# Performance work log

Hardware: AMD Instinct MI355X
Metric: run time of the kernel (lower is better)

Reference implementation:

```python
import jax, jax.numpy as jnp
import numpy as np

B, H0, W0, C, NH, WS, SHIFT = 32, 48, 48, 384, 12, 12, 6
N = WS * WS
TAB = 2 * WS - 1  # 23


def _window_partition(x, ws):
    b, h, w, c = x.shape
    x = x.reshape(b, h // ws, ws, w // ws, ws, c)
    return x.transpose(0, 1, 3, 2, 4, 5).reshape(-1, ws, ws, c)


def _window_reverse(win, ws, h, w):
    b = win.shape[0] // (h * w // ws // ws)
    x = win.reshape(b, h // ws, w // ws, ws, ws, -1)
    return x.transpose(0, 1, 3, 2, 4, 5).reshape(b, h, w, -1)


def _ln(y, g, b):
    m = y.mean(-1, keepdims=True)
    v = y.var(-1, keepdims=True)
    return (y - m) * jax.lax.rsqrt(v + 1e-5) * g + b


def setup_inputs() -> dict:
    key = jax.random.key(0)
    ks = jax.random.split(key, 12)
    s = 0.02
    # relative coords table, normalized to [-1, 1]
    rng = np.arange(-(WS - 1), WS, dtype=np.float32) / (WS - 1)
    table = np.stack(np.meshgrid(rng, rng, indexing='ij'), axis=-1)[None]  # (1,23,23,2)
    # relative position index
    ch, cw = np.meshgrid(np.arange(WS), np.arange(WS), indexing='ij')
    coords = np.stack([ch, cw]).reshape(2, -1)
    rel = coords[:, :, None] - coords[:, None, :] + (WS - 1)
    rpi = (rel[0] * TAB + rel[1]).astype(np.int32)  # (N,N)
    # shifted-window attention mask
    img = np.zeros((1, H0, W0, 1), dtype=np.float32)
    cnt = 0
    sl = (slice(0, -WS), slice(-WS, -SHIFT), slice(-SHIFT, None))
    for hs in sl:
        for ws_ in sl:
            img[:, hs, ws_, :] = cnt
            cnt += 1
    mw = img.reshape(1, H0 // WS, WS, W0 // WS, WS, 1).transpose(0, 1, 3, 2, 4, 5).reshape(-1, N)
    diff = mw[:, None, :] - mw[:, :, None]
    attn_mask = np.where(diff != 0, -100.0, 0.0).astype(np.float32)  # (nW,N,N)
    Ch = C * 4
    return {
        'x': jax.random.normal(ks[0], (B, H0 * W0, C), jnp.float32),
        'relative_coords_table': jnp.asarray(table),
        'relative_position_index': jnp.asarray(rpi),
        'attn_mask': jnp.asarray(attn_mask),
        'qkv_w': jax.random.normal(ks[1], (C, 3 * C), jnp.float32) * s,
        'q_bias': jnp.zeros((C,), jnp.float32),
        'v_bias': jnp.zeros((C,), jnp.float32),
        'logit_scale': jnp.log(10.0 * jnp.ones((NH, 1, 1), jnp.float32)),
        'cpb_w1': jax.random.normal(ks[2], (2, 512), jnp.float32) * s,
        'cpb_b1': jnp.zeros((512,), jnp.float32),
        'cpb_w2': jax.random.normal(ks[3], (512, NH), jnp.float32) * s,
        'proj_w': jax.random.normal(ks[4], (C, C), jnp.float32) * s,
        'proj_b': jnp.zeros((C,), jnp.float32),
        'norm1_g': jnp.ones((C,), jnp.float32),
        'norm1_b': jnp.zeros((C,), jnp.float32),
        'norm2_g': jnp.ones((C,), jnp.float32),
        'norm2_b': jnp.zeros((C,), jnp.float32),
        'fc1_w': jax.random.normal(ks[5], (C, Ch), jnp.float32) * s,
        'fc1_b': jnp.zeros((Ch,), jnp.float32),
        'fc2_w': jax.random.normal(ks[6], (Ch, C), jnp.float32) * s,
        'fc2_b': jnp.zeros((C,), jnp.float32),
        'H': H0,
        'W': W0,
    }


def reference(x, relative_coords_table, relative_position_index, attn_mask,
              qkv_w, q_bias, v_bias, logit_scale, cpb_w1, cpb_b1, cpb_w2,
              proj_w, proj_b, norm1_g, norm1_b, norm2_g, norm2_b,
              fc1_w, fc1_b, fc2_w, fc2_b, H, W):
    b, L, c = x.shape
    hd = c // NH
    shortcut = x
    x4 = x.reshape(b, H, W, c)
    shifted = jnp.roll(x4, (-SHIFT, -SHIFT), axis=(1, 2))
    xw = _window_partition(shifted, WS).reshape(-1, N, c)  # (B_, N, C)
    qkv_bias = jnp.concatenate([q_bias, jnp.zeros_like(q_bias), v_bias])
    qkv = xw @ qkv_w + qkv_bias
    qkv = qkv.reshape(-1, N, 3, NH, hd).transpose(2, 0, 3, 1, 4)  # (3,B_,h,N,d)
    q, k, v = qkv[0], qkv[1], qkv[2]
    qn = q / jnp.maximum(jnp.linalg.norm(q, axis=-1, keepdims=True), 1e-12)
    kn = k / jnp.maximum(jnp.linalg.norm(k, axis=-1, keepdims=True), 1e-12)
    attn = jnp.einsum('bhnd,bhmd->bhnm', qn, kn)
    scale = jnp.exp(jnp.minimum(logit_scale, jnp.log(100.0)))  # clamp max=log(1/0.01)
    attn = attn * scale
    tab = jax.nn.relu(relative_coords_table @ cpb_w1 + cpb_b1) @ cpb_w2  # (1,23,23,h)
    tab = tab.reshape(-1, NH)
    bias = tab[relative_position_index.reshape(-1)].reshape(N, N, NH).transpose(2, 0, 1)
    bias = 16.0 * jax.nn.sigmoid(bias)
    attn = attn + bias[None]
    nW = attn_mask.shape[0]
    attn = attn.reshape(b, nW, NH, N, N) + attn_mask[None, :, None]
    attn = jax.nn.softmax(attn.reshape(-1, NH, N, N), axis=-1)
    out = jnp.einsum('bhnm,bhmd->bhnd', attn, v).transpose(0, 2, 1, 3).reshape(-1, N, c)
    out = out @ proj_w + proj_b
    out = _window_reverse(out.reshape(-1, WS, WS, c), WS, H, W)
    x4 = jnp.roll(out, (SHIFT, SHIFT), axis=(1, 2)).reshape(b, H * W, c)
    x = shortcut + _ln(x4, norm1_g, norm1_b)
    h = jax.nn.gelu(x @ fc1_w + fc1_b, approximate=False) @ fc2_w + fc2_b
    x = x + _ln(h, norm2_g, norm2_b)
    return x
```

## Files before the change

### kernel.cpp

```cpp
#include <hip/hip_runtime.h>


typedef unsigned int uint32;
typedef unsigned short u16;
typedef __attribute__((ext_vector_type(4))) float f32x4;
typedef __attribute__((ext_vector_type(8))) __bf16 bf16x8;

static __device__ __forceinline__ u16 f2bf(float f) {
    union { float f; uint32 u; } v; v.f = f;
    uint32 r = v.u + 0x7fffu + ((v.u >> 16) & 1u);
    return (u16)(r >> 16);
}
static __device__ __forceinline__ float bf2f(u16 h) {
    union { uint32 u; float f; } v; v.u = ((uint32)h) << 16; return v.f;
}
static __device__ __forceinline__ uint32 pack2(float a, float b) {
    return (uint32)f2bf(a) | ((uint32)f2bf(b) << 16);
}
static __device__ __forceinline__ float blo(uint32 u){ union{uint32 u;float f;}v; v.u=u<<16; return v.f; }
static __device__ __forceinline__ float bhi(uint32 u){ union{uint32 u;float f;}v; v.u=u&0xffff0000u; return v.f; }

typedef __attribute__((address_space(1))) const void gas_void;
typedef __attribute__((address_space(3))) void las_void;
static __device__ __forceinline__ void glds16(const void* g, void* l) {
    __builtin_amdgcn_global_load_lds((gas_void*)g, (las_void*)l, 16, 0, 0);
}

#define SWZ(c, row) ((c) ^ ((((row) >> 1) & 3) << 3))

#define VMCNT(N) asm volatile("s_waitcnt vmcnt(" #N ")" ::: "memory")
#define BARM() do { asm volatile("" ::: "memory"); __builtin_amdgcn_s_barrier(); asm volatile("" ::: "memory"); } while (0)

static __device__ __forceinline__ float fast_gelu(float x) {
    float z = x * 0.70710678118654752f;
    float az = fabsf(z);
    float t = __builtin_amdgcn_rcpf(fmaf(0.3275911f, az, 1.0f));
    float p = t * (0.254829592f + t * (-0.284496736f + t * (1.421413741f
              + t * (-1.453152027f + t * 1.061405429f))));
    float e = __expf(-z * z);
    float er = copysignf(fmaf(-p, e, 1.0f), z);
    return 0.5f * x * (1.0f + er);
}


__global__ void wt_convert(const float* __restrict__ W, u16* __restrict__ WT, int K, int N) {
    long idx = (long)blockIdx.x * 256 + threadIdx.x;
    long tot = (long)K * N;
    if (idx >= tot) return;
    int n = (int)(idx / K), k = (int)(idx - (long)n * K);
    WT[(long)n * K + SWZ(k, n)] = f2bf(W[(long)k * N + n]);
}

__global__ void build_qkv_bias(const float* __restrict__ qb, const float* __restrict__ vb,
                               float* __restrict__ outb) {
    int c = blockIdx.x * 256 + threadIdx.x;
    if (c >= 1152) return;
    outb[c] = (c < 384) ? qb[c] : ((c < 768) ? 0.f : vb[c - 768]);
}

__global__ void cpb_tab(const float* __restrict__ table, const float* __restrict__ w1,
                        const float* __restrict__ b1, const float* __restrict__ w2,
                        float* __restrict__ tab) {
    __shared__ float hid[512];
    int e = blockIdx.x;
    float tx = table[e * 2 + 0], ty = table[e * 2 + 1];
    for (int u = threadIdx.x; u < 512; u += 256)
        hid[u] = fmaxf(tx * w1[u] + ty * w1[512 + u] + b1[u], 0.f);
    __syncthreads();
    if (threadIdx.x < 12) {
        float s = 0.f;
        for (int u = 0; u < 512; ++u) s += hid[u] * w2[u * 12 + threadIdx.x];
        tab[e * 12 + threadIdx.x] = s;
    }
}

__global__ void cpb_bias(const float* __restrict__ tab, const int* __restrict__ rpi,
                         float* __restrict__ bias16) {
    int idx = blockIdx.x * 256 + threadIdx.x;
    if (idx >= 12 * 144 * 144) return;
    int h = idx / 20736, ij = idx - h * 20736;
    float t = tab[rpi[ij] * 12 + h];
    bias16[idx] = 16.f / (1.f + __expf(-t));
}

__global__ void gather_xbf(const float* __restrict__ x, u16* __restrict__ xw) {
    int idx = blockIdx.x * 256 + threadIdx.x;
    if (idx >= 73728 * 48) return;
    int row = idx / 48, c = (idx - row * 48) * 8;
    int win = row / 144, n = row - win * 144;
    int b = win >> 4, wi = win & 15;
    int r = n / 12, cc = n - r * 12;
    int sh = ((wi >> 2) * 12 + r + 6) % 48;
    int sw = ((wi & 3) * 12 + cc + 6) % 48;
    long src = ((long)(b * 2304 + sh * 48 + sw)) * 384 + c;
    float4 f0 = *(const float4*)(x + src);
    float4 f1 = *(const float4*)(x + src + 4);
    uint4 o;
    o.x = pack2(f0.x, f0.y); o.y = pack2(f0.z, f0.w);
    o.z = pack2(f1.x, f1.y); o.w = pack2(f1.z, f1.w);
    *(uint4*)(xw + (long)row * 384 + SWZ(c, row)) = o;
}


enum { EPI_QKV = 0, EPI_PLAIN = 1, EPI_GELU = 2 };

template<int EPI, bool OSWZ, int NK>
__global__ __launch_bounds__(256, 2) void gemm_k(
    const u16* __restrict__ Ag, const u16* __restrict__ Bg,
    const float* __restrict__ bias, u16* __restrict__ outp,
    int N, int ntn)
{
    constexpr int K = NK * 32;
    extern __shared__ u16 lds[];
    u16* As = lds;
    u16* Bs = lds + 24576;

    const int tid = threadIdx.x, lane = tid & 63, wid = tid >> 6;
    const int qq = gridDim.x >> 3;
    const int wg = (blockIdx.x & 7) * qq + (blockIdx.x >> 3);
    const int mIdx = wg / ntn, nIdx = wg - mIdx * ntn;
    const int m0 = mIdx << 8, n0 = nIdx << 7;

    const int wrow = wid << 6;
    const int fr = lane & 15, gsel = lane >> 4;

    const int srow = (wid << 4) + (lane >> 2);
    const int scol = (lane & 3) << 3;
    const u16* aP[4];
    const u16* bP[2];
#pragma unroll
    for (int q = 0; q < 4; ++q) aP[q] = Ag + (long)(m0 + (q << 6) + srow) * K + scol;
#pragma unroll
    for (int q = 0; q < 2; ++q) bP[q] = Bg + (long)(n0 + (q << 6) + srow) * K + scol;

    auto stage = [&](int buf, int kt) {
#pragma unroll
        for (int q = 0; q < 4; ++q)
            glds16(aP[q] + (kt << 5), &As[buf * 8192 + ((q << 6) + (wid << 4)) * 32]);
#pragma unroll
        for (int q = 0; q < 2; ++q)
            glds16(bP[q] + (kt << 5), &Bs[buf * 4096 + ((q << 6) + (wid << 4)) * 32]);
    };

    int arow[4], acol[4], brow[8], bcol[8];
#pragma unroll
    for (int i = 0; i < 4; ++i) {
        arow[i] = wrow + i * 16 + fr;
        acol[i] = (gsel ^ ((arow[i] >> 1) & 3)) << 3;
    }
#pragma unroll
    for (int j = 0; j < 8; ++j) {
        brow[j] = j * 16 + fr;
        bcol[j] = (gsel ^ ((brow[j] >> 1) & 3)) << 3;
    }

    f32x4 acc[4][8];
    const f32x4 zero4 = {0.f, 0.f, 0.f, 0.f};
#pragma unroll
    for (int i = 0; i < 4; ++i)
#pragma unroll
        for (int j = 0; j < 8; ++j) acc[i][j] = zero4;

    auto compute = [&](int buf) {
        const u16* pa = As + buf * 8192;
        const u16* pb = Bs + buf * 4096;
        bf16x8 af[4], bg[8];
#pragma unroll
        for (int i = 0; i < 4; ++i) af[i] = *(const bf16x8*)&pa[arow[i] * 32 + acol[i]];
#pragma unroll
        for (int j = 0; j < 8; ++j) bg[j] = *(const bf16x8*)&pb[brow[j] * 32 + bcol[j]];
#pragma unroll
        for (int i = 0; i < 4; ++i)
#pragma unroll
            for (int j = 0; j < 8; ++j)
                acc[i][j] = __builtin_amdgcn_mfma_f32_16x16x32_bf16(af[i], bg[j], acc[i][j], 0, 0, 0);
    };

    stage(0, 0);
    stage(1, 1);
#define GITER(KT, BC, BN_) \
    VMCNT(6); BARM(); stage(BN_, (KT) + 2); compute(BC);
    for (int g = 0; g < (NK - 1) / 3; ++g) {
        const int kb = g * 3;
        GITER(kb + 0, 0, 2);
        GITER(kb + 1, 1, 0);
        GITER(kb + 2, 2, 1);
    }
#undef GITER
    VMCNT(6); BARM(); stage(2, NK - 1); compute(0);
    VMCNT(6); BARM(); compute(1);
    VMCNT(0); BARM(); compute(2);

    const int rbase = gsel << 2;
    if constexpr (EPI == EPI_QKV) {
        long coloff[8];
        float bv[8];
#pragma unroll
        for (int j = 0; j < 8; ++j) {
            int gn0 = n0 + j * 16;
            int which = gn0 / 384;
            int c = gn0 - which * 384;
            coloff[j] = (long)(which * 12 + (c >> 5)) * 4608 + (c & 31) + fr;
            bv[j] = bias[gn0 + fr];
        }
#pragma unroll
        for (int i = 0; i < 4; ++i) {
            long rowoff[4];
#pragma unroll
            for (int r = 0; r < 4; ++r) {
                int gm = m0 + wrow + i * 16 + rbase + r;
                int win = gm / 144, n = gm - win * 144;
                rowoff[r] = (long)win * 165888 + n * 32;
            }
#pragma unroll
            for (int j = 0; j < 8; ++j)
#pragma unroll
                for (int r = 0; r < 4; ++r)
                    outp[rowoff[r] + coloff[j]] = f2bf(acc[i][j][r] + bv[j]);
        }
    } else {
        float bv[8];
#pragma unroll
        for (int j = 0; j < 8; ++j) bv[j] = bias[n0 + j * 16 + fr];
#pragma unroll
        for (int i = 0; i < 4; ++i) {
#pragma unroll
            for (int r = 0; r < 4; ++r) {
                const int gm = m0 + wrow + i * 16 + rbase + r;
                u16* orow = outp + (long)gm * N;
                const int sx = OSWZ ? (((gm >> 1) & 3) << 3) : 0;
#pragma unroll
                for (int j = 0; j < 8; ++j) {
                    const int gn = n0 + j * 16 + fr;
                    float v = acc[i][j][r] + bv[j];
                    if constexpr (EPI == EPI_GELU) v = fast_gelu(v);
                    orow[gn ^ sx] = f2bf(v);
                }
            }
        }
    }
}


__global__ __launch_bounds__(192) void attn_k(
    const u16* __restrict__ qkv,
    const float* __restrict__ bias16,
    const float* __restrict__ mask,
    const float* __restrict__ lsc,
    u16* __restrict__ attn_o)
{
    __shared__ __align__(16) u16 KL[144][40];
    __shared__ __align__(16) u16 VT[32][168];
    __shared__ __align__(16) u16 PL[3][16][168];
    const int blk = blockIdx.x;
    const int win = blk / 12, head = blk - win * 12;
    const int tid = threadIdx.x, lane = tid & 63, wid = tid >> 6;
    const long base = ((long)win * 36 + head) * 4608;
    const u16* Qp = qkv + base;
    const u16* Kp = qkv + base + 12 * 4608;
    const u16* Vp = qkv + base + 24 * 4608;
    const float scale = __expf(fminf(lsc[head], 4.6051701859880914f));

    if (tid < 144) {
        const uint4* s = (const uint4*)(Kp + tid * 32);
        uint4 uu[4] = { s[0], s[1], s[2], s[3] };
        float f[32];
#pragma unroll
        for (int q = 0; q < 4; ++q) {
            f[q*8+0]=blo(uu[q].x); f[q*8+1]=bhi(uu[q].x);
            f[q*8+2]=blo(uu[q].y); f[q*8+3]=bhi(uu[q].y);
            f[q*8+4]=blo(uu[q].z); f[q*8+5]=bhi(uu[q].z);
            f[q*8+6]=blo(uu[q].w); f[q*8+7]=bhi(uu[q].w);
        }
        float ss = 0.f;
#pragma unroll
        for (int i = 0; i < 32; ++i) ss += f[i] * f[i];
        float inv = 1.f / fmaxf(sqrtf(ss), 1e-12f);
        uint32 pk[16];
#pragma unroll
        for (int i = 0; i < 16; ++i) pk[i] = pack2(f[2*i] * inv, f[2*i+1] * inv);
        uint4* d = (uint4*)&KL[tid][0];
        d[0] = make_uint4(pk[0], pk[1], pk[2], pk[3]);
        d[1] = make_uint4(pk[4], pk[5], pk[6], pk[7]);
        d[2] = make_uint4(pk[8], pk[9], pk[10], pk[11]);
        d[3] = make_uint4(pk[12], pk[13], pk[14], pk[15]);
        const uint4* sv = (const uint4*)(Vp + tid * 32);
        uint4 vv[4] = { sv[0], sv[1], sv[2], sv[3] };
        u16 vs[32];
#pragma unroll
        for (int q = 0; q < 4; ++q) {
            vs[q*8+0] = (u16)(vv[q].x & 0xffffu); vs[q*8+1] = (u16)(vv[q].x >> 16);
            vs[q*8+2] = (u16)(vv[q].y & 0xffffu); vs[q*8+3] = (u16)(vv[q].y >> 16);
            vs[q*8+4] = (u16)(vv[q].z & 0xffffu); vs[q*8+5] = (u16)(vv[q].z >> 16);
            vs[q*8+6] = (u16)(vv[q].w & 0xffffu); vs[q*8+7] = (u16)(vv[q].w >> 16);
        }
#pragma unroll
        for (int d2 = 0; d2 < 32; ++d2) VT[d2][tid] = vs[d2];
    }
    for (int idx = tid; idx < 512; idx += 192) VT[idx >> 4][144 + (idx & 15)] = 0;
    __syncthreads();

    const int fr = lane & 15, fk = (lane >> 4) << 3, rb = (lane >> 4) << 2;
    const int wim = win & 15;
    const f32x4 zero4 = {0.f, 0.f, 0.f, 0.f};

    for (int s = wid; s < 9; s += 3) {
        const uint4 qu = *(const uint4*)(Qp + (s * 16 + fr) * 32 + fk);
        float qf[8];
        qf[0]=blo(qu.x); qf[1]=bhi(qu.x); qf[2]=blo(qu.y); qf[3]=bhi(qu.y);
        qf[4]=blo(qu.z); qf[5]=bhi(qu.z); qf[6]=blo(qu.w); qf[7]=bhi(qu.w);
        float ss = 0.f;
#pragma unroll
        for (int i = 0; i < 8; ++i) ss += qf[i] * qf[i];
        ss += __shfl_xor(ss, 16);
        ss += __shfl_xor(ss, 32);
        float qinv = scale / fmaxf(sqrtf(ss), 1e-12f);
        union { uint32 u[4]; bf16x8 v; } cv;
#pragma unroll
        for (int i = 0; i < 4; ++i) cv.u[i] = pack2(qf[2*i] * qinv, qf[2*i+1] * qinv);
        bf16x8 aq = cv.v;

        f32x4 sacc[9];
#pragma unroll
        for (int jt = 0; jt < 9; ++jt) sacc[jt] = zero4;
#pragma unroll
        for (int jt = 0; jt < 9; ++jt) {
            bf16x8 bk = *(const bf16x8*)&KL[jt * 16 + fr][fk];
            sacc[jt] = __builtin_amdgcn_mfma_f32_16x16x32_bf16(aq, bk, sacc[jt], 0, 0, 0);
        }
        float mx[4] = {-1e30f, -1e30f, -1e30f, -1e30f};
#pragma unroll
        for (int jt = 0; jt < 9; ++jt) {
            int gj = jt * 16 + fr;
#pragma unroll
            for (int r = 0; r < 4; ++r) {
                int gi = s * 16 + rb + r;
                float v = sacc[jt][r] + bias16[(head * 144 + gi) * 144 + gj]
                                      + mask[(wim * 144 + gi) * 144 + gj];
                sacc[jt][r] = v;
                mx[r] = fmaxf(mx[r], v);
            }
        }
#pragma unroll
        for (int r = 0; r < 4; ++r) {
#pragma unroll
            for (int o = 1; o < 16; o <<= 1) mx[r] = fmaxf(mx[r], __shfl_xor(mx[r], o));
        }
        float sm[4] = {0.f, 0.f, 0.f, 0.f};
#pragma unroll
        for (int jt = 0; jt < 9; ++jt)
#pragma unroll
            for (int r = 0; r < 4; ++r) {
                float e = __expf(sacc[jt][r] - mx[r]);
                sacc[jt][r] = e;
                sm[r] += e;
            }
#pragma unroll
        for (int r = 0; r < 4; ++r) {
#pragma unroll
            for (int o = 1; o < 16; o <<= 1) sm[r] += __shfl_xor(sm[r], o);
            sm[r] = 1.f / sm[r];
        }
#pragma unroll
        for (int jt = 0; jt < 9; ++jt)
#pragma unroll
            for (int r = 0; r < 4; ++r)
                PL[wid][rb + r][jt * 16 + fr] = f2bf(sacc[jt][r]);
#pragma unroll
        for (int r = 0; r < 4; ++r) PL[wid][rb + r][144 + fr] = 0;

        f32x4 oa0 = zero4, oa1 = zero4;
#pragma unroll
        for (int kt = 0; kt < 5; ++kt) {
            bf16x8 ap  = *(const bf16x8*)&PL[wid][fr][kt * 32 + fk];
            bf16x8 bv0 = *(const bf16x8*)&VT[fr][kt * 32 + fk];
            bf16x8 bv1 = *(const bf16x8*)&VT[16 + fr][kt * 32 + fk];
            oa0 = __builtin_amdgcn_mfma_f32_16x16x32_bf16(ap, bv0, oa0, 0, 0, 0);
            oa1 = __builtin_amdgcn_mfma_f32_16x16x32_bf16(ap, bv1, oa1, 0, 0, 0);
        }
#pragma unroll
        for (int r = 0; r < 4; ++r) {
            long row = (long)win * 144 + s * 16 + rb + r;
            int c0 = head * 32 + fr, c1 = head * 32 + 16 + fr;
            attn_o[row * 384 + SWZ(c0, row)] = f2bf(oa0[r] * sm[r]);
            attn_o[row * 384 + SWZ(c1, row)] = f2bf(oa1[r] * sm[r]);
        }
    }
}


__global__ __launch_bounds__(256) void ln1_k(
    const u16* __restrict__ pin, const float* __restrict__ x,
    const float* __restrict__ g, const float* __restrict__ bb,
    u16* __restrict__ y1b)
{
    const int token = blockIdx.x * 4 + (threadIdx.x >> 6);
    const int lane = threadIdx.x & 63;
    int b = token / 2304, hw = token - b * 2304;
    int h = hw / 48, w = hw - h * 48;
    int sh = h + 42; if (sh >= 48) sh -= 48;
    int sw = w + 42; if (sw >= 48) sw -= 48;
    int wh = sh / 12, r = sh - wh * 12;
    int ww = sw / 12, cc = sw - ww * 12;
    long srow = (long)(b * 16 + wh * 4 + ww) * 144 + r * 12 + cc;
    const u16* src = pin + srow * 384;
    float v[6];
    {
        const ushort2* s2 = (const ushort2*)src;
#pragma unroll
        for (int i = 0; i < 3; ++i) {
            ushort2 p = s2[lane * 3 + i];
            v[i * 2] = bf2f(p.x); v[i * 2 + 1] = bf2f(p.y);
        }
    }
    float s1 = 0.f, s2 = 0.f;
#pragma unroll
    for (int i = 0; i < 6; ++i) { s1 += v[i]; s2 += v[i] * v[i]; }
#pragma unroll
    for (int o = 1; o < 64; o <<= 1) { s1 += __shfl_xor(s1, o); s2 += __shfl_xor(s2, o); }
    float mean = s1 * (1.f / 384.f);
    float var = s2 * (1.f / 384.f) - mean * mean;
    float rs = rsqrtf(var + 1e-5f);
    const float* rr = x + (long)token * 384;
    u16* oo = y1b + (long)token * 384;
#pragma unroll
    for (int i = 0; i < 6; ++i) {
        int c = lane * 6 + i;
        oo[SWZ(c, token)] = f2bf(rr[c] + (v[i] - mean) * rs * g[c] + bb[c]);
    }
}

__global__ __launch_bounds__(256) void ln2_k(
    const u16* __restrict__ t2, const u16* __restrict__ y1b,
    const float* __restrict__ g, const float* __restrict__ bb,
    float* __restrict__ outp)
{
    const int token = blockIdx.x * 4 + (threadIdx.x >> 6);
    const int lane = threadIdx.x & 63;
    const u16* src = t2 + (long)token * 384;
    float v[6];
    {
        const ushort2* s2 = (const ushort2*)src;
#pragma unroll
        for (int i = 0; i < 3; ++i) {
            ushort2 p = s2[lane * 3 + i];
            v[i * 2] = bf2f(p.x); v[i * 2 + 1] = bf2f(p.y);
        }
    }
    float s1 = 0.f, s2 = 0.f;
#pragma unroll
    for (int i = 0; i < 6; ++i) { s1 += v[i]; s2 += v[i] * v[i]; }
#pragma unroll
    for (int o = 1; o < 64; o <<= 1) { s1 += __shfl_xor(s1, o); s2 += __shfl_xor(s2, o); }
    float mean = s1 * (1.f / 384.f);
    float var = s2 * (1.f / 384.f) - mean * mean;
    float rs = rsqrtf(var + 1e-5f);
    const u16* rr = y1b + (long)token * 384;
    float* oo = outp + (long)token * 384;
#pragma unroll
    for (int i = 0; i < 6; ++i) {
        int c = lane * 6 + i;
        oo[c] = bf2f(rr[SWZ(c, token)]) + (v[i] - mean) * rs * g[c] + bb[c];
    }
}


extern "C" void kernel_launch(void* const* d_in, const int* in_sizes, int n_in,
                              void* d_out, int out_size, void* d_ws, size_t ws_size,
                              hipStream_t stream) {
    (void)in_sizes; (void)n_in; (void)out_size; (void)ws_size;
    const float* x      = (const float*)d_in[0];
    const float* table  = (const float*)d_in[1];
    const int*   rpi    = (const int*)d_in[2];
    const float* mask   = (const float*)d_in[3];
    const float* qkv_w  = (const float*)d_in[4];
    const float* q_bias = (const float*)d_in[5];
    const float* v_bias = (const float*)d_in[6];
    const float* lsc    = (const float*)d_in[7];
    const float* cpb_w1 = (const float*)d_in[8];
    const float* cpb_b1 = (const float*)d_in[9];
    const float* cpb_w2 = (const float*)d_in[10];
    const float* proj_w = (const float*)d_in[11];
    const float* proj_b = (const float*)d_in[12];
    const float* n1g    = (const float*)d_in[13];
    const float* n1b    = (const float*)d_in[14];
    const float* n2g    = (const float*)d_in[15];
    const float* n2b    = (const float*)d_in[16];
    const float* fc1_w  = (const float*)d_in[17];
    const float* fc1_b  = (const float*)d_in[18];
    const float* fc2_w  = (const float*)d_in[19];
    const float* fc2_b  = (const float*)d_in[20];
    float* outp = (float*)d_out;

    char* ws = (char*)d_ws;
    const size_t offA    = 0;
    const size_t offB    = 226492416;
    const size_t offC    = offB + 56623104;
    const size_t offBias = offC + 56623104;
    const size_t offTab  = offBias + 995328;
    const size_t offQW   = offTab + 25600;
    const size_t offPW   = offQW + 884736;
    const size_t offF1   = offPW + 294912;
    const size_t offF2   = offF1 + 1179648;
    const size_t offQB   = offF2 + 1179648;

    u16*   qkvb    = (u16*)(ws + offA);
    u16*   proj_o  = (u16*)(ws + offA);
    u16*   hbuf    = (u16*)(ws + offA);
    u16*   attn_o  = (u16*)(ws + offB);
    u16*   t2      = (u16*)(ws + offB);
    u16*   xw      = (u16*)(ws + offC);
    u16*   y1b     = (u16*)(ws + offC);
    float* bias16  = (float*)(ws + offBias);
    float* tab     = (float*)(ws + offTab);
    u16*   qkv_wT  = (u16*)(ws + offQW);
    u16*   proj_wT = (u16*)(ws + offPW);
    u16*   fc1_wT  = (u16*)(ws + offF1);
    u16*   fc2_wT  = (u16*)(ws + offF2);
    float* qkvbias = (float*)(ws + offQB);

    hipFuncSetAttribute((const void*)&gemm_k<EPI_QKV, false, 12>,
                        hipFuncAttributeMaxDynamicSharedMemorySize, 73728);
    hipFuncSetAttribute((const void*)&gemm_k<EPI_PLAIN, false, 12>,
                        hipFuncAttributeMaxDynamicSharedMemorySize, 73728);
    hipFuncSetAttribute((const void*)&gemm_k<EPI_GELU, true, 12>,
                        hipFuncAttributeMaxDynamicSharedMemorySize, 73728);
    hipFuncSetAttribute((const void*)&gemm_k<EPI_PLAIN, false, 48>,
                        hipFuncAttributeMaxDynamicSharedMemorySize, 73728);

    wt_convert<<<(384 * 1152 + 255) / 256, 256, 0, stream>>>(qkv_w, qkv_wT, 384, 1152);
    wt_convert<<<(384 * 384 + 255) / 256, 256, 0, stream>>>(proj_w, proj_wT, 384, 384);
    wt_convert<<<(384 * 1536 + 255) / 256, 256, 0, stream>>>(fc1_w, fc1_wT, 384, 1536);
    wt_convert<<<(1536 * 384 + 255) / 256, 256, 0, stream>>>(fc2_w, fc2_wT, 1536, 384);
    build_qkv_bias<<<5, 256, 0, stream>>>(q_bias, v_bias, qkvbias);
    cpb_tab<<<529, 256, 0, stream>>>(table, cpb_w1, cpb_b1, cpb_w2, tab);
    cpb_bias<<<(12 * 144 * 144 + 255) / 256, 256, 0, stream>>>(tab, rpi, bias16);
    gather_xbf<<<(73728 * 48 + 255) / 256, 256, 0, stream>>>(x, xw);

    gemm_k<EPI_QKV, false, 12><<<288 * 9, 256, 73728, stream>>>(xw, qkv_wT, qkvbias, qkvb, 1152, 9);

    attn_k<<<6144, 192, 0, stream>>>(qkvb, bias16, mask, lsc, attn_o);

    gemm_k<EPI_PLAIN, false, 12><<<288 * 3, 256, 73728, stream>>>(attn_o, proj_wT, proj_b, proj_o, 384, 3);

    ln1_k<<<18432, 256, 0, stream>>>(proj_o, x, n1g, n1b, y1b);

    gemm_k<EPI_GELU, true, 12><<<288 * 12, 256, 73728, stream>>>(y1b, fc1_wT, fc1_b, hbuf, 1536, 12);

    gemm_k<EPI_PLAIN, false, 48><<<288 * 3, 256, 73728, stream>>>(hbuf, fc2_wT, fc2_b, t2, 384, 3);

    ln2_k<<<18432, 256, 0, stream>>>(t2, y1b, n2g, n2b, outp);
}
```

Baseline: 737.4 us.

## Switch GEMM to static double-buffered LDS, simplify QKV layout, vectorize LayerNorms, tanh-GELU

Shrinks the GEMM's shared memory from three dynamic stages to two static buffers and raises launch bounds to 3 blocks per CU, aiming for more occupancy at the cost of less load/compute overlap (full vmcnt(0) waits). The QKV GEMM now writes a plain row-major output, and the attention kernel reads with a strided layout instead of the head-major scatter. LayerNorm kernels use vectorized loads and stores. GELU is replaced by a sigmoid-based tanh approximation, which departs from the exact erf GELU.

```diff
diff --git a/kernel.cpp b/kernel.cpp
--- a/kernel.cpp
+++ b/kernel.cpp
@@ -32,14 +32,11 @@
 #define BARM() do { asm volatile("" ::: "memory"); __builtin_amdgcn_s_barrier(); asm volatile("" ::: "memory"); } while (0)
 
 static __device__ __forceinline__ float fast_gelu(float x) {
-    float z = x * 0.70710678118654752f;
-    float az = fabsf(z);
-    float t = __builtin_amdgcn_rcpf(fmaf(0.3275911f, az, 1.0f));
-    float p = t * (0.254829592f + t * (-0.284496736f + t * (1.421413741f
-              + t * (-1.453152027f + t * 1.061405429f))));
-    float e = __expf(-z * z);
-    float er = copysignf(fmaf(-p, e, 1.0f), z);
-    return 0.5f * x * (1.0f + er);
+    float x2 = x * x;
+    float w = x * fmaf(0.0713548162f, x2, 1.5957691216f);
+    float e = __expf(w);
+    float r = __builtin_amdgcn_rcpf(e + 1.0f);
+    return fmaf(-x, r, x);
 }
 
 
@@ -102,18 +99,17 @@
 }
 
 
-enum { EPI_QKV = 0, EPI_PLAIN = 1, EPI_GELU = 2 };
+enum { EPI_PLAIN = 1, EPI_GELU = 2 };
 
 template<int EPI, bool OSWZ, int NK>
-__global__ __launch_bounds__(256, 2) void gemm_k(
+__global__ __launch_bounds__(256, 3) void gemm_k(
     const u16* __restrict__ Ag, const u16* __restrict__ Bg,
     const float* __restrict__ bias, u16* __restrict__ outp,
     int N, int ntn)
 {
     constexpr int K = NK * 32;
-    extern __shared__ u16 lds[];
-    u16* As = lds;
-    u16* Bs = lds + 24576;
+    __shared__ __align__(16) u16 As[2][8192];
+    __shared__ __align__(16) u16 Bs[2][4096];
 
     const int tid = threadIdx.x, lane = tid & 63, wid = tid >> 6;
     const int qq = gridDim.x >> 3;
@@ -136,10 +132,10 @@
     auto stage = [&](int buf, int kt) {
 #pragma unroll
         for (int q = 0; q < 4; ++q)
-            glds16(aP[q] + (kt << 5), &As[buf * 8192 + ((q << 6) + (wid << 4)) * 32]);
+            glds16(aP[q] + (kt << 5), &As[buf][((q << 6) + (wid << 4)) * 32]);
 #pragma unroll
         for (int q = 0; q < 2; ++q)
-            glds16(bP[q] + (kt << 5), &Bs[buf * 4096 + ((q << 6) + (wid << 4)) * 32]);
+            glds16(bP[q] + (kt << 5), &Bs[buf][((q << 6) + (wid << 4)) * 32]);
     };
 
     int arow[4], acol[4], brow[8], bcol[8];
@@ -162,8 +158,8 @@
         for (int j = 0; j < 8; ++j) acc[i][j] = zero4;
 
     auto compute = [&](int buf) {
-        const u16* pa = As + buf * 8192;
-        const u16* pb = Bs + buf * 4096;
+        const u16* pa = &As[buf][0];
+        const u16* pb = &Bs[buf][0];
         bf16x8 af[4], bg[8];
 #pragma unroll
         for (int i = 0; i < 4; ++i) af[i] = *(const bf16x8*)&pa[arow[i] * 32 + acol[i]];
@@ -177,65 +173,33 @@
     };
 
     stage(0, 0);
-    stage(1, 1);
-#define GITER(KT, BC, BN_) \
-    VMCNT(6); BARM(); stage(BN_, (KT) + 2); compute(BC);
-    for (int g = 0; g < (NK - 1) / 3; ++g) {
-        const int kb = g * 3;
-        GITER(kb + 0, 0, 2);
-        GITER(kb + 1, 1, 0);
-        GITER(kb + 2, 2, 1);
-    }
-#undef GITER
-    VMCNT(6); BARM(); stage(2, NK - 1); compute(0);
-    VMCNT(6); BARM(); compute(1);
-    VMCNT(0); BARM(); compute(2);
+#pragma unroll
+    for (int g = 0; g < NK / 2; ++g) {
+        VMCNT(0); BARM();
+        stage(1, 2 * g + 1);
+        compute(0);
+        VMCNT(0); BARM();
+        if (g + 1 < NK / 2) stage(0, 2 * g + 2);
+        compute(1);
+    }
 
     const int rbase = gsel << 2;
-    if constexpr (EPI == EPI_QKV) {
-        long coloff[8];
-        float bv[8];
-#pragma unroll
-        for (int j = 0; j < 8; ++j) {
-            int gn0 = n0 + j * 16;
-            int which = gn0 / 384;
-            int c = gn0 - which * 384;
-            coloff[j] = (long)(which * 12 + (c >> 5)) * 4608 + (c & 31) + fr;
-            bv[j] = bias[gn0 + fr];
-        }
-#pragma unroll
-        for (int i = 0; i < 4; ++i) {
-            long rowoff[4];
-#pragma unroll
-            for (int r = 0; r < 4; ++r) {
-                int gm = m0 + wrow + i * 16 + rbase + r;
-                int win = gm / 144, n = gm - win * 144;
-                rowoff[r] = (long)win * 165888 + n * 32;
-            }
-#pragma unroll
-            for (int j = 0; j < 8; ++j)
-#pragma unroll
-                for (int r = 0; r < 4; ++r)
-                    outp[rowoff[r] + coloff[j]] = f2bf(acc[i][j][r] + bv[j]);
-        }
-    } else {
-        float bv[8];
-#pragma unroll
-        for (int j = 0; j < 8; ++j) bv[j] = bias[n0 + j * 16 + fr];
-#pragma unroll
-        for (int i = 0; i < 4; ++i) {
-#pragma unroll
-            for (int r = 0; r < 4; ++r) {
-                const int gm = m0 + wrow + i * 16 + rbase + r;
-                u16* orow = outp + (long)gm * N;
-                const int sx = OSWZ ? (((gm >> 1) & 3) << 3) : 0;
-#pragma unroll
-                for (int j = 0; j < 8; ++j) {
-                    const int gn = n0 + j * 16 + fr;
-                    float v = acc[i][j][r] + bv[j];
-                    if constexpr (EPI == EPI_GELU) v = fast_gelu(v);
-                    orow[gn ^ sx] = f2bf(v);
-                }
+    float bv[8];
+#pragma unroll
+    for (int j = 0; j < 8; ++j) bv[j] = bias[n0 + j * 16 + fr];
+#pragma unroll
+    for (int i = 0; i < 4; ++i) {
+#pragma unroll
+        for (int r = 0; r < 4; ++r) {
+            const int gm = m0 + wrow + i * 16 + rbase + r;
+            u16* orow = outp + (long)gm * N;
+            const int sx = OSWZ ? (((gm >> 1) & 3) << 3) : 0;
+#pragma unroll
+            for (int j = 0; j < 8; ++j) {
+                const int gn = n0 + j * 16 + fr;
+                float v = acc[i][j][r] + bv[j];
+                if constexpr (EPI == EPI_GELU) v = fast_gelu(v);
+                orow[gn ^ sx] = f2bf(v);
             }
         }
     }
@@ -255,14 +219,13 @@
     const int blk = blockIdx.x;
     const int win = blk / 12, head = blk - win * 12;
     const int tid = threadIdx.x, lane = tid & 63, wid = tid >> 6;
-    const long base = ((long)win * 36 + head) * 4608;
-    const u16* Qp = qkv + base;
-    const u16* Kp = qkv + base + 12 * 4608;
-    const u16* Vp = qkv + base + 24 * 4608;
+    const u16* Qp = qkv + (long)win * 144 * 1152 + head * 32;
+    const u16* Kp = Qp + 384;
+    const u16* Vp = Qp + 768;
     const float scale = __expf(fminf(lsc[head], 4.6051701859880914f));
 
     if (tid < 144) {
-        const uint4* s = (const uint4*)(Kp + tid * 32);
+        const uint4* s = (const uint4*)(Kp + (long)tid * 1152);
         uint4 uu[4] = { s[0], s[1], s[2], s[3] };
         float f[32];
 #pragma unroll
@@ -284,7 +247,7 @@
         d[1] = make_uint4(pk[4], pk[5], pk[6], pk[7]);
         d[2] = make_uint4(pk[8], pk[9], pk[10], pk[11]);
         d[3] = make_uint4(pk[12], pk[13], pk[14], pk[15]);
-        const uint4* sv = (const uint4*)(Vp + tid * 32);
+        const uint4* sv = (const uint4*)(Vp + (long)tid * 1152);
         uint4 vv[4] = { sv[0], sv[1], sv[2], sv[3] };
         u16 vs[32];
 #pragma unroll
@@ -305,7 +268,7 @@
     const f32x4 zero4 = {0.f, 0.f, 0.f, 0.f};
 
     for (int s = wid; s < 9; s += 3) {
-        const uint4 qu = *(const uint4*)(Qp + (s * 16 + fr) * 32 + fk);
+        const uint4 qu = *(const uint4*)(Qp + (long)(s * 16 + fr) * 1152 + fk);
         float qf[8];
         qf[0]=blo(qu.x); qf[1]=bhi(qu.x); qf[2]=blo(qu.y); qf[3]=bhi(qu.y);
         qf[4]=blo(qu.z); qf[5]=bhi(qu.z); qf[6]=blo(qu.w); qf[7]=bhi(qu.w);
@@ -404,15 +367,10 @@
     int ww = sw / 12, cc = sw - ww * 12;
     long srow = (long)(b * 16 + wh * 4 + ww) * 144 + r * 12 + cc;
     const u16* src = pin + srow * 384;
-    float v[6];
-    {
-        const ushort2* s2 = (const ushort2*)src;
-#pragma unroll
-        for (int i = 0; i < 3; ++i) {
-            ushort2 p = s2[lane * 3 + i];
-            v[i * 2] = bf2f(p.x); v[i * 2 + 1] = bf2f(p.y);
-        }
-    }
+    const int c0 = lane * 4, c1 = 256 + lane * 2;
+    uint2 p0 = *(const uint2*)(src + c0);
+    uint32 p1 = *(const uint32*)(src + c1);
+    float v[6] = { blo(p0.x), bhi(p0.x), blo(p0.y), bhi(p0.y), blo(p1), bhi(p1) };
     float s1 = 0.f, s2 = 0.f;
 #pragma unroll
     for (int i = 0; i < 6; ++i) { s1 += v[i]; s2 += v[i] * v[i]; }
@@ -421,13 +379,24 @@
     float mean = s1 * (1.f / 384.f);
     float var = s2 * (1.f / 384.f) - mean * mean;
     float rs = rsqrtf(var + 1e-5f);
-    const float* rr = x + (long)token * 384;
+    const float* xx = x + (long)token * 384;
+    float4 r0 = *(const float4*)(xx + c0);
+    float2 r1 = *(const float2*)(xx + c1);
+    float4 g0 = *(const float4*)(g + c0);
+    float2 g1 = *(const float2*)(g + c1);
+    float4 b0 = *(const float4*)(bb + c0);
+    float2 b1 = *(const float2*)(bb + c1);
+    float o0 = r0.x + (v[0] - mean) * rs * g0.x + b0.x;
+    float o1 = r0.y + (v[1] - mean) * rs * g0.y + b0.y;
+    float o2 = r0.z + (v[2] - mean) * rs * g0.z + b0.z;
+    float o3 = r0.w + (v[3] - mean) * rs * g0.w + b0.w;
+    float o4 = r1.x + (v[4] - mean) * rs * g1.x + b1.x;
+    float o5 = r1.y + (v[5] - mean) * rs * g1.y + b1.y;
     u16* oo = y1b + (long)token * 384;
-#pragma unroll
-    for (int i = 0; i < 6; ++i) {
-        int c = lane * 6 + i;
-        oo[SWZ(c, token)] = f2bf(rr[c] + (v[i] - mean) * rs * g[c] + bb[c]);
-    }
+    const int sx = ((token >> 1) & 3) << 3;
+    uint2 w0; w0.x = pack2(o0, o1); w0.y = pack2(o2, o3);
+    *(uint2*)(oo + (c0 ^ sx)) = w0;
+    *(uint32*)(oo + (c1 ^ sx)) = pack2(o4, o5);
 }
 
 __global__ __launch_bounds__(256) void ln2_k(
@@ -437,16 +406,11 @@
 {
     const int token = blockIdx.x * 4 + (threadIdx.x >> 6);
     const int lane = threadIdx.x & 63;
+    const int c0 = lane * 4, c1 = 256 + lane * 2;
     const u16* src = t2 + (long)token * 384;
-    float v[6];
-    {
-        const ushort2* s2 = (const ushort2*)src;
-#pragma unroll
-        for (int i = 0; i < 3; ++i) {
-            ushort2 p = s2[lane * 3 + i];
-            v[i * 2] = bf2f(p.x); v[i * 2 + 1] = bf2f(p.y);
-        }
-    }
+    uint2 p0 = *(const uint2*)(src + c0);
+    uint32 p1 = *(const uint32*)(src + c1);
+    float v[6] = { blo(p0.x), bhi(p0.x), blo(p0.y), bhi(p0.y), blo(p1), bhi(p1) };
     float s1 = 0.f, s2 = 0.f;
 #pragma unroll
     for (int i = 0; i < 6; ++i) { s1 += v[i]; s2 += v[i] * v[i]; }
@@ -456,12 +420,24 @@
     float var = s2 * (1.f / 384.f) - mean * mean;
     float rs = rsqrtf(var + 1e-5f);
     const u16* rr = y1b + (long)token * 384;
+    const int sx = ((token >> 1) & 3) << 3;
+    uint2 q0 = *(const uint2*)(rr + (c0 ^ sx));
+    uint32 q1 = *(const uint32*)(rr + (c1 ^ sx));
+    float4 g0 = *(const float4*)(g + c0);
+    float2 g1 = *(const float2*)(g + c1);
+    float4 b0 = *(const float4*)(bb + c0);
+    float2 b1 = *(const float2*)(bb + c1);
     float* oo = outp + (long)token * 384;
-#pragma unroll
-    for (int i = 0; i < 6; ++i) {
-        int c = lane * 6 + i;
-        oo[c] = bf2f(rr[SWZ(c, token)]) + (v[i] - mean) * rs * g[c] + bb[c];
-    }
+    float4 w0;
+    w0.x = blo(q0.x) + (v[0] - mean) * rs * g0.x + b0.x;
+    w0.y = bhi(q0.x) + (v[1] - mean) * rs * g0.y + b0.y;
+    w0.z = blo(q0.y) + (v[2] - mean) * rs * g0.z + b0.z;
+    w0.w = bhi(q0.y) + (v[3] - mean) * rs * g0.w + b0.w;
+    float2 w1;
+    w1.x = blo(q1) + (v[4] - mean) * rs * g1.x + b1.x;
+    w1.y = bhi(q1) + (v[5] - mean) * rs * g1.y + b1.y;
+    *(float4*)(oo + c0) = w0;
+    *(float2*)(oo + c1) = w1;
 }
 
 
@@ -519,15 +495,6 @@
     u16*   fc2_wT  = (u16*)(ws + offF2);
     float* qkvbias = (float*)(ws + offQB);
 
-    hipFuncSetAttribute((const void*)&gemm_k<EPI_QKV, false, 12>,
-                        hipFuncAttributeMaxDynamicSharedMemorySize, 73728);
-    hipFuncSetAttribute((const void*)&gemm_k<EPI_PLAIN, false, 12>,
-                        hipFuncAttributeMaxDynamicSharedMemorySize, 73728);
-    hipFuncSetAttribute((const void*)&gemm_k<EPI_GELU, true, 12>,
-                        hipFuncAttributeMaxDynamicSharedMemorySize, 73728);
-    hipFuncSetAttribute((const void*)&gemm_k<EPI_PLAIN, false, 48>,
-                        hipFuncAttributeMaxDynamicSharedMemorySize, 73728);
-
     wt_convert<<<(384 * 1152 + 255) / 256, 256, 0, stream>>>(qkv_w, qkv_wT, 384, 1152);
     wt_convert<<<(384 * 384 + 255) / 256, 256, 0, stream>>>(proj_w, proj_wT, 384, 384);
     wt_convert<<<(384 * 1536 + 255) / 256, 256, 0, stream>>>(fc1_w, fc1_wT, 384, 1536);
@@ -537,17 +504,17 @@
     cpb_bias<<<(12 * 144 * 144 + 255) / 256, 256, 0, stream>>>(tab, rpi, bias16);
     gather_xbf<<<(73728 * 48 + 255) / 256, 256, 0, stream>>>(x, xw);
 
-    gemm_k<EPI_QKV, false, 12><<<288 * 9, 256, 73728, stream>>>(xw, qkv_wT, qkvbias, qkvb, 1152, 9);
+    gemm_k<EPI_PLAIN, false, 12><<<288 * 9, 256, 0, stream>>>(xw, qkv_wT, qkvbias, qkvb, 1152, 9);
 
     attn_k<<<6144, 192, 0, stream>>>(qkvb, bias16, mask, lsc, attn_o);
 
-    gemm_k<EPI_PLAIN, false, 12><<<288 * 3, 256, 73728, stream>>>(attn_o, proj_wT, proj_b, proj_o, 384, 3);
+    gemm_k<EPI_PLAIN, false, 12><<<288 * 3, 256, 0, stream>>>(attn_o, proj_wT, proj_b, proj_o, 384, 3);
 
     ln1_k<<<18432, 256, 0, stream>>>(proj_o, x, n1g, n1b, y1b);
 
-    gemm_k<EPI_GELU, true, 12><<<288 * 12, 256, 73728, stream>>>(y1b, fc1_wT, fc1_b, hbuf, 1536, 12);
-
-    gemm_k<EPI_PLAIN, false, 48><<<288 * 3, 256, 73728, stream>>>(hbuf, fc2_wT, fc2_b, t2, 384, 3);
+    gemm_k<EPI_GELU, true, 12><<<288 * 12, 256, 0, stream>>>(y1b, fc1_wT, fc1_b, hbuf, 1536, 12);
+
+    gemm_k<EPI_PLAIN, false, 48><<<288 * 3, 256, 0, stream>>>(hbuf, fc2_wT, fc2_b, t2, 384, 3);
 
     ln2_k<<<18432, 256, 0, stream>>>(t2, y1b, n2g, n2b, outp);
 }
```

Result: slower. 1.986 ms (+169.3%).
